# Performance work log

Measured on AMD Instinct MI355X. Metric: run time of the kernel, lower is better.

## Reference

```python
import jax, jax.numpy as jnp
import numpy as np

CLIP_MAX = 1.0 / 1e-06  # torch.clip(1/d, max=1/1e-6)


def setup_inputs() -> dict:
    key = jax.random.key(0)
    k1, k2 = jax.random.split(key)
    base_features = jax.random.normal(k1, (4096, 512), dtype=jnp.float32)
    target_features = jax.random.normal(k2, (8192, 512), dtype=jnp.float32)
    return {"base_features": base_features, "target_features": target_features}


def _pairwise_euclidean(x, y):
    # Same math as sqrt(sum((x[:,None,:]-y[None,:,:])**2, -1)) but computed
    # via the expanded form to avoid materializing the (N,M,D) intermediate.
    x2 = jnp.sum(x * x, axis=1, keepdims=True)          # [N,1]
    y2 = jnp.sum(y * y, axis=1, keepdims=True).T        # [1,M]
    xy = x @ y.T                                        # [N,M]
    sq = jnp.maximum(x2 + y2 - 2.0 * xy, 0.0)
    return jnp.sqrt(sq)


def reference(base_features, target_features):
    # distance == 'euclidean' branch of SimilarityCalculatorFeatureOnly.forward
    dist = _pairwise_euclidean(base_features, target_features)   # [N,M]
    similarity = jnp.minimum(1.0 / dist, CLIP_MAX)                # clip at 1e6
    return (base_features, similarity)
```

## Files before the change

kernel.cpp:

```cpp
#include <hip/hip_runtime.h>
#include <hip/hip_bf16.h>
#include <stdint.h>

typedef short bf16x8 __attribute__((ext_vector_type(8)));
typedef float f32x4 __attribute__((ext_vector_type(4)));

#define D  512
#define NB 4096
#define NT 8192

__device__ __forceinline__ unsigned short f2bf(float f) {
    __hip_bfloat16 h = __float2bfloat16(f);
    return *reinterpret_cast<unsigned short*>(&h);
}

__global__ __launch_bounds__(256) void prep_kernel(
    const float* __restrict__ x, const float* __restrict__ y,
    unsigned short* __restrict__ xb, unsigned short* __restrict__ yb,
    float* __restrict__ x2, float* __restrict__ y2, float* __restrict__ copy)
{
    const int grow = blockIdx.x * 4 + (threadIdx.x >> 6);
    const int lane = threadIdx.x & 63;
    const bool isX = grow < NB;
    const int row  = isX ? grow : grow - NB;
    const float* src = isX ? x : y;
    unsigned short* dst = isX ? xb : yb;
    float* norms = isX ? x2 : y2;

    const float4* rp = reinterpret_cast<const float4*>(src + (size_t)row * D);
    float4 v0 = rp[lane * 2];
    float4 v1 = rp[lane * 2 + 1];
    if (isX) {
        float4* cp = reinterpret_cast<float4*>(copy + (size_t)row * D);
        cp[lane * 2]     = v0;
        cp[lane * 2 + 1] = v1;
    }
    float s = v0.x*v0.x + v0.y*v0.y + v0.z*v0.z + v0.w*v0.w
            + v1.x*v1.x + v1.y*v1.y + v1.z*v1.z + v1.w*v1.w;
    union { unsigned short h[8]; int4 v; } u;
    u.h[0] = f2bf(v0.x); u.h[1] = f2bf(v0.y); u.h[2] = f2bf(v0.z); u.h[3] = f2bf(v0.w);
    u.h[4] = f2bf(v1.x); u.h[5] = f2bf(v1.y); u.h[6] = f2bf(v1.z); u.h[7] = f2bf(v1.w);
    reinterpret_cast<int4*>(dst + (size_t)row * D)[lane] = u.v;
    #pragma unroll
    for (int off = 32; off > 0; off >>= 1) s += __shfl_xor(s, off);
    if (lane == 0) norms[row] = s;
}

__global__ __launch_bounds__(256, 2) void gemm_sim_kernel(
    const unsigned short* __restrict__ X, const unsigned short* __restrict__ Y,
    const float* __restrict__ x2, const float* __restrict__ y2,
    float* __restrict__ out)
{
    __shared__ alignas(16) unsigned short lds[36864];

    const int t    = threadIdx.x;
    const int lane = t & 63;
    const int w    = t >> 6;

    const int bid = blockIdx.x;
    const int xcd = bid & 7;
    const int idx = bid >> 3;
    const int rowBase = ((xcd >> 2) * 16 + (idx & 15)) * 128;
    const int colBase = ((xcd & 3) * 8 + (idx >> 4)) * 256;

    const int swz = ((t & 3) ^ ((t >> 3) & 3)) * 8;
    const unsigned short* gA = X + (size_t)(rowBase + (t >> 2)) * D + swz;
    const unsigned short* gB = Y + (size_t)(colBase + (t >> 2)) * D + swz;

    const int cread = ((lane >> 4) ^ ((lane >> 1) & 3)) * 8;
    const int aoff = (lane & 15) * 32 + cread;
    const int boff = 4096 + (w * 64 + (lane & 15)) * 32 + cread;

    f32x4 acc[8][4] = {};
    bf16x8 bfr[4];

#define STAGE_A(BUF, KT) do { \
    _Pragma("unroll") \
    for (int L = 0; L < 2; ++L) \
        __builtin_amdgcn_global_load_lds( \
            (const __attribute__((address_space(1))) void*)(gA + (size_t)L * 64 * D + (KT) * 32), \
            (__attribute__((address_space(3))) void*)(lds + (BUF) * 12288 + t * 8 + L * 2048), 16, 0, 0); \
} while (0)

#define STAGE_B(BUF, KT) do { \
    _Pragma("unroll") \
    for (int L = 0; L < 4; ++L) \
        __builtin_amdgcn_global_load_lds( \
            (const __attribute__((address_space(1))) void*)(gB + (size_t)L * 64 * D + (KT) * 32), \
            (__attribute__((address_space(3))) void*)(lds + (BUF) * 12288 + 4096 + t * 8 + L * 2048), 16, 0, 0); \
} while (0)

#define PHASE(BUF, MH, STG, CKPT) do { \
    bf16x8 _a[4]; \
    if ((MH) == 0) { \
        _Pragma("unroll") \
        for (int n = 0; n < 4; ++n) \
            bfr[n] = *(const bf16x8*)(lds + (BUF) * 12288 + boff + n * 512); \
    } \
    _Pragma("unroll") \
    for (int m = 0; m < 4; ++m) \
        _a[m] = *(const bf16x8*)(lds + (BUF) * 12288 + aoff + (MH) * 2048 + m * 512); \
    STG; \
    __builtin_amdgcn_s_barrier(); \
    asm volatile("s_waitcnt lgkmcnt(0)" ::: "memory"); \
    __builtin_amdgcn_s_setprio(1); \
    _Pragma("unroll") \
    for (int m = 0; m < 4; ++m) { \
        _Pragma("unroll") \
        for (int n = 0; n < 4; ++n) \
            acc[(MH) * 4 + m][n] = __builtin_amdgcn_mfma_f32_16x16x32_bf16(_a[m], bfr[n], acc[(MH) * 4 + m][n], 0, 0, 0); \
    } \
    __builtin_amdgcn_s_setprio(0); \
    CKPT; \
    __builtin_amdgcn_s_barrier(); \
} while (0)

    STAGE_A(0, 0); STAGE_B(0, 0);
    STAGE_A(1, 1); STAGE_B(1, 1);
    asm volatile("s_waitcnt vmcnt(6)" ::: "memory");
    __builtin_amdgcn_s_barrier();

#pragma unroll
    for (int kt = 0; kt < 16; ++kt) {
        PHASE((kt % 3), 0,
              if (kt + 2 < 16) STAGE_A(((kt + 2) % 3), kt + 2),
              ((void)0));
        PHASE((kt % 3), 1,
              if (kt + 2 < 16) STAGE_B(((kt + 2) % 3), kt + 2),
              if (kt < 14)      { asm volatile("s_waitcnt vmcnt(6)" ::: "memory"); }
              else if (kt == 14){ asm volatile("s_waitcnt vmcnt(0)" ::: "memory"); });
    }
#undef PHASE
#undef STAGE_A
#undef STAGE_B

    const int col0 = colBase + w * 64 + (lane & 15);
    const int row0 = rowBase + ((lane >> 4) << 2);
    #pragma unroll
    for (int mi = 0; mi < 8; ++mi) {
        const int rbase = row0 + (mi >> 2) * 64 + (mi & 3) * 16;
        #pragma unroll
        for (int q = 0; q < 4; ++q) {
            const int grow = rbase + q;
            const float xn = x2[grow];
            float* orow = out + (size_t)grow * NT;
            #pragma unroll
            for (int n = 0; n < 4; ++n) {
                const int gcol = col0 + n * 16;
                float sq = fmaxf(xn + y2[gcol] - 2.0f * acc[mi][n][q], 0.0f);
                orow[gcol] = fminf(rsqrtf(sq), 1.0e6f);
            }
        }
    }
}

extern "C" void kernel_launch(void* const* d_in, const int* in_sizes, int n_in,
                              void* d_out, int out_size, void* d_ws, size_t ws_size,
                              hipStream_t stream)
{
    const float* x = (const float*)d_in[0];
    const float* y = (const float*)d_in[1];
    float* out = (float*)d_out;
    char* ws = (char*)d_ws;

    unsigned short* xb = (unsigned short*)ws;
    unsigned short* yb = (unsigned short*)(ws + (4u << 20));
    float* x2 = (float*)(ws + (12u << 20));
    float* y2 = (float*)(ws + (12u << 20) + 4 * NB);

    prep_kernel<<<(NB + NT) / 4, 256, 0, stream>>>(x, y, xb, yb, x2, y2, out);
    gemm_sim_kernel<<<1024, 256, 0, stream>>>(xb, yb, x2, y2, out + (size_t)NB * D);
}
```

Measured before the change: 60.64 us.

## Warp-specialize GEMM to overlap similarity output stores with next tile's MFMA

Each block now processes four 128x256 output tiles in sequence, using 256 blocks of 384 threads. Four compute waves run the MFMA K-loop, and two extra waves stream the previous tile's results from LDS to global memory with nontemporal stores. Compute waves write the clipped inverse distances into LDS as bf16 and preload the row and column norms into registers once. The aim is to hide the large fp32 output write behind the matrix multiply, at the cost of lower occupancy, more LDS use and rounding the output to bf16 precision.

```diff
diff --git a/kernel.cpp b/kernel.cpp
--- a/kernel.cpp
+++ b/kernel.cpp
@@ -4,6 +4,7 @@
 
 typedef short bf16x8 __attribute__((ext_vector_type(8)));
 typedef float f32x4 __attribute__((ext_vector_type(4)));
+typedef float f32x2 __attribute__((ext_vector_type(2)));
 
 #define D  512
 #define NB 4096
@@ -46,33 +47,55 @@
     if (lane == 0) norms[row] = s;
 }
 
-__global__ __launch_bounds__(256, 2) void gemm_sim_kernel(
+__global__ __launch_bounds__(384, 1) void gemm_sim_kernel(
     const unsigned short* __restrict__ X, const unsigned short* __restrict__ Y,
     const float* __restrict__ x2, const float* __restrict__ y2,
     float* __restrict__ out)
 {
-    __shared__ alignas(16) unsigned short lds[36864];
+    __shared__ alignas(16) unsigned short lds[69632];
 
     const int t    = threadIdx.x;
     const int lane = t & 63;
     const int w    = t >> 6;
+    const bool isCompute = (w < 4);
 
     const int bid = blockIdx.x;
     const int xcd = bid & 7;
     const int idx = bid >> 3;
-    const int rowBase = ((xcd >> 2) * 16 + (idx & 15)) * 128;
-    const int colBase = ((xcd & 3) * 8 + (idx >> 4)) * 256;
+    const int rowBase   = ((xcd & 1) * 16 + (idx & 15)) * 128;
+    const int colGroup0 = ((xcd >> 1) * 2 + (idx >> 4)) * 1024;
 
     const int swz = ((t & 3) ^ ((t >> 3) & 3)) * 8;
-    const unsigned short* gA = X + (size_t)(rowBase + (t >> 2)) * D + swz;
-    const unsigned short* gB = Y + (size_t)(colBase + (t >> 2)) * D + swz;
+    const unsigned short* gA = X + (size_t)(rowBase   + (t >> 2)) * D + swz;
+    const unsigned short* gB = Y + (size_t)(colGroup0 + (t >> 2)) * D + swz;
 
     const int cread = ((lane >> 4) ^ ((lane >> 1) & 3)) * 8;
     const int aoff = (lane & 15) * 32 + cread;
     const int boff = 4096 + (w * 64 + (lane & 15)) * 32 + cread;
 
+    const int col_l0 = w * 64 + (lane & 15);
+    const int row_l0 = (lane >> 4) << 2;
+    unsigned short* xf = lds + 36864;
+    const int g = (w - 4) * 64 + lane;
+
     f32x4 acc[8][4] = {};
-    bf16x8 bfr[4];
+
+    float x2v[32], y2v[16];
+    if (isCompute) {
+        #pragma unroll
+        for (int mi = 0; mi < 8; ++mi)
+            #pragma unroll
+            for (int q = 0; q < 4; ++q)
+                x2v[mi * 4 + q] = x2[rowBase + row_l0 + (mi >> 2) * 64 + (mi & 3) * 16 + q];
+        #pragma unroll
+        for (int tl = 0; tl < 4; ++tl)
+            #pragma unroll
+            for (int n = 0; n < 4; ++n)
+                y2v[tl * 4 + n] = y2[colGroup0 + tl * 256 + col_l0 + n * 16];
+    }
+
+#define BAR() do { asm volatile("" ::: "memory"); __builtin_amdgcn_s_barrier(); \
+                   asm volatile("" ::: "memory"); } while (0)
 
 #define STAGE_A(BUF, KT) do { \
     _Pragma("unroll") \
@@ -82,76 +105,118 @@
             (__attribute__((address_space(3))) void*)(lds + (BUF) * 12288 + t * 8 + L * 2048), 16, 0, 0); \
 } while (0)
 
-#define STAGE_B(BUF, KT) do { \
+#define STAGE_B(BUF, KT, TL) do { \
     _Pragma("unroll") \
     for (int L = 0; L < 4; ++L) \
         __builtin_amdgcn_global_load_lds( \
-            (const __attribute__((address_space(1))) void*)(gB + (size_t)L * 64 * D + (KT) * 32), \
+            (const __attribute__((address_space(1))) void*)(gB + (size_t)(TL) * 256 * D + (size_t)L * 64 * D + (KT) * 32), \
             (__attribute__((address_space(3))) void*)(lds + (BUF) * 12288 + 4096 + t * 8 + L * 2048), 16, 0, 0); \
 } while (0)
 
-#define PHASE(BUF, MH, STG, CKPT) do { \
-    bf16x8 _a[4]; \
-    if ((MH) == 0) { \
+#define KTBODY(TL, KT) do { \
+    if (isCompute) { \
+        bf16x8 _a[2][4], _b[4]; \
         _Pragma("unroll") \
         for (int n = 0; n < 4; ++n) \
-            bfr[n] = *(const bf16x8*)(lds + (BUF) * 12288 + boff + n * 512); \
+            _b[n] = *(const bf16x8*)(lds + ((KT) % 3) * 12288 + boff + n * 512); \
+        _Pragma("unroll") \
+        for (int h = 0; h < 2; ++h) \
+            _Pragma("unroll") \
+            for (int m = 0; m < 4; ++m) \
+                _a[h][m] = *(const bf16x8*)(lds + ((KT) % 3) * 12288 + aoff + h * 2048 + m * 512); \
+        if ((KT) + 2 < 16) { \
+            STAGE_A(((KT) + 2) % 3, (KT) + 2); \
+            STAGE_B(((KT) + 2) % 3, (KT) + 2, TL); \
+        } \
+        __builtin_amdgcn_s_setprio(1); \
+        _Pragma("unroll") \
+        for (int h = 0; h < 2; ++h) \
+            _Pragma("unroll") \
+            for (int m = 0; m < 4; ++m) \
+                _Pragma("unroll") \
+                for (int n = 0; n < 4; ++n) \
+                    acc[h * 4 + m][n] = __builtin_amdgcn_mfma_f32_16x16x32_bf16( \
+                        _a[h][m], _b[n], acc[h * 4 + m][n], 0, 0, 0); \
+        __builtin_amdgcn_s_setprio(0); \
+        __builtin_amdgcn_sched_barrier(0); \
+        if ((KT) < 14)       { asm volatile("s_waitcnt vmcnt(6)" ::: "memory"); } \
+        else if ((KT) == 14) { asm volatile("s_waitcnt vmcnt(0)" ::: "memory"); } \
+    } else if ((TL) > 0) { \
+        const uint32_t* xfu = (const uint32_t*)xf; \
+        _Pragma("unroll") \
+        for (int j = 0; j < 8; ++j) { \
+            const int r = (KT) * 8 + j; \
+            uint32_t u = xfu[r * 128 + g]; \
+            f32x2 v; \
+            v.x = __uint_as_float(u << 16); \
+            v.y = __uint_as_float(u & 0xffff0000u); \
+            __builtin_nontemporal_store(v, \
+                (f32x2*)(out + (size_t)(rowBase + r) * NT + colGroup0 + ((TL) - 1) * 256 + 2 * g)); \
+        } \
     } \
-    _Pragma("unroll") \
-    for (int m = 0; m < 4; ++m) \
-        _a[m] = *(const bf16x8*)(lds + (BUF) * 12288 + aoff + (MH) * 2048 + m * 512); \
-    STG; \
-    __builtin_amdgcn_s_barrier(); \
-    asm volatile("s_waitcnt lgkmcnt(0)" ::: "memory"); \
-    __builtin_amdgcn_s_setprio(1); \
-    _Pragma("unroll") \
-    for (int m = 0; m < 4; ++m) { \
-        _Pragma("unroll") \
-        for (int n = 0; n < 4; ++n) \
-            acc[(MH) * 4 + m][n] = __builtin_amdgcn_mfma_f32_16x16x32_bf16(_a[m], bfr[n], acc[(MH) * 4 + m][n], 0, 0, 0); \
+    BAR(); \
+} while (0)
+
+#define TILE(TL) do { \
+    BAR();   \
+    KTBODY(TL, 0);  KTBODY(TL, 1);  KTBODY(TL, 2);  KTBODY(TL, 3); \
+    KTBODY(TL, 4);  KTBODY(TL, 5);  KTBODY(TL, 6);  KTBODY(TL, 7); \
+    KTBODY(TL, 8);  KTBODY(TL, 9);  KTBODY(TL, 10); KTBODY(TL, 11); \
+    KTBODY(TL, 12); KTBODY(TL, 13); KTBODY(TL, 14); KTBODY(TL, 15); \
+    if (isCompute) { \
+        if ((TL) < 3) { \
+            STAGE_A(0, 0); STAGE_B(0, 0, (TL) + 1); \
+            STAGE_A(1, 1); STAGE_B(1, 1, (TL) + 1); \
+        } \
+        _Pragma("unroll") \
+        for (int mi = 0; mi < 8; ++mi) { \
+            const int rb = row_l0 + (mi >> 2) * 64 + (mi & 3) * 16; \
+            _Pragma("unroll") \
+            for (int q = 0; q < 4; ++q) { \
+                _Pragma("unroll") \
+                for (int n = 0; n < 4; ++n) { \
+                    float sq = fmaxf(x2v[mi * 4 + q] + y2v[(TL) * 4 + n] \
+                                     - 2.0f * acc[mi][n][q], 0.0f); \
+                    xf[(rb + q) * 256 + col_l0 + n * 16] = \
+                        f2bf(fminf(rsqrtf(sq), 1.0e6f)); \
+                } \
+            } \
+        } \
+        _Pragma("unroll") \
+        for (int mi = 0; mi < 8; ++mi) \
+            _Pragma("unroll") \
+            for (int n = 0; n < 4; ++n) \
+                acc[mi][n] = (f32x4){0.f, 0.f, 0.f, 0.f}; \
+        asm volatile("s_waitcnt lgkmcnt(0)" ::: "memory"); \
+        if ((TL) < 3) { asm volatile("s_waitcnt vmcnt(6)" ::: "memory"); } \
     } \
-    __builtin_amdgcn_s_setprio(0); \
-    CKPT; \
-    __builtin_amdgcn_s_barrier(); \
-} while (0)
-
-    STAGE_A(0, 0); STAGE_B(0, 0);
-    STAGE_A(1, 1); STAGE_B(1, 1);
-    asm volatile("s_waitcnt vmcnt(6)" ::: "memory");
-    __builtin_amdgcn_s_barrier();
-
-#pragma unroll
-    for (int kt = 0; kt < 16; ++kt) {
-        PHASE((kt % 3), 0,
-              if (kt + 2 < 16) STAGE_A(((kt + 2) % 3), kt + 2),
-              ((void)0));
-        PHASE((kt % 3), 1,
-              if (kt + 2 < 16) STAGE_B(((kt + 2) % 3), kt + 2),
-              if (kt < 14)      { asm volatile("s_waitcnt vmcnt(6)" ::: "memory"); }
-              else if (kt == 14){ asm volatile("s_waitcnt vmcnt(0)" ::: "memory"); });
-    }
-#undef PHASE
+} while (0)
+
+    if (isCompute) {
+        STAGE_A(0, 0); STAGE_B(0, 0, 0);
+        STAGE_A(1, 1); STAGE_B(1, 1, 0);
+        asm volatile("s_waitcnt vmcnt(6)" ::: "memory");
+    }
+
+    TILE(0); TILE(1); TILE(2); TILE(3);
+    BAR();
+
+    if (!isCompute) {
+        const uint32_t* xfu = (const uint32_t*)xf;
+        for (int r = 0; r < 128; ++r) {
+            uint32_t u = xfu[r * 128 + g];
+            f32x2 v;
+            v.x = __uint_as_float(u << 16);
+            v.y = __uint_as_float(u & 0xffff0000u);
+            __builtin_nontemporal_store(v,
+                (f32x2*)(out + (size_t)(rowBase + r) * NT + colGroup0 + 768 + 2 * g));
+        }
+    }
+#undef TILE
+#undef KTBODY
 #undef STAGE_A
 #undef STAGE_B
-
-    const int col0 = colBase + w * 64 + (lane & 15);
-    const int row0 = rowBase + ((lane >> 4) << 2);
-    #pragma unroll
-    for (int mi = 0; mi < 8; ++mi) {
-        const int rbase = row0 + (mi >> 2) * 64 + (mi & 3) * 16;
-        #pragma unroll
-        for (int q = 0; q < 4; ++q) {
-            const int grow = rbase + q;
-            const float xn = x2[grow];
-            float* orow = out + (size_t)grow * NT;
-            #pragma unroll
-            for (int n = 0; n < 4; ++n) {
-                const int gcol = col0 + n * 16;
-                float sq = fmaxf(xn + y2[gcol] - 2.0f * acc[mi][n][q], 0.0f);
-                orow[gcol] = fminf(rsqrtf(sq), 1.0e6f);
-            }
-        }
-    }
+#undef BAR
 }
 
 extern "C" void kernel_launch(void* const* d_in, const int* in_sizes, int n_in,
@@ -169,5 +234,5 @@
     float* y2 = (float*)(ws + (12u << 20) + 4 * NB);
 
     prep_kernel<<<(NB + NT) / 4, 256, 0, stream>>>(x, y, xb, yb, x2, y2, out);
-    gemm_sim_kernel<<<1024, 256, 0, stream>>>(xb, yb, x2, y2, out + (size_t)NB * D);
-}
+    gemm_sim_kernel<<<256, 384, 0, stream>>>(xb, yb, x2, y2, out + (size_t)NB * D);
+}
```

Measured after the change: 79.18 us. 1.31x slower.
